# Kernel tuning notes

Hardware: AMD Instinct MI355X
Metric: run time of the kernel (lower is better)

The kernel has to match this reference:

```python
import jax, jax.numpy as jnp
import numpy as np

B, S, D_IN = 2, 2048, 2048
D_OUT, H, RD, L = 2048, 16, 64, 512
HD = D_OUT // H  # 128
ROPE_BASE = 10000.0
EPS = 1e-6


def _rmsnorm(x, w):
    # RMSNorm over last dim
    ms = jnp.mean(jnp.square(x), axis=-1, keepdims=True)
    return x * jax.lax.rsqrt(ms + EPS) * w


def _apply_rope(x, offset):
    # x: [B, H, T, RD]; GPT-NeoX style rotary embedding
    T, rd = x.shape[-2], x.shape[-1]
    pos = (offset + jnp.arange(T)).astype(jnp.float32)  # [T]
    inv_freq = 1.0 / (ROPE_BASE ** (jnp.arange(0, rd, 2, dtype=jnp.float32) / rd))  # [rd/2]
    ang = pos[:, None] * inv_freq[None, :]              # [T, rd/2]
    cos = jnp.cos(jnp.concatenate([ang, ang], axis=-1))  # [T, rd]
    sin = jnp.sin(jnp.concatenate([ang, ang], axis=-1))
    x1, x2 = jnp.split(x, 2, axis=-1)
    rot = jnp.concatenate([-x2, x1], axis=-1)
    return x * cos + rot * sin


def setup_inputs() -> dict:
    key = jax.random.key(0)
    ks = jax.random.split(key, 8)
    sc = 0.02
    return {
        "x": jax.random.normal(ks[0], (B, S, D_IN), jnp.float32),
        "W_DKV": jax.random.normal(ks[1], (L, D_IN), jnp.float32) * sc,
        "W_KRope": jax.random.normal(ks[2], (H * RD, D_IN), jnp.float32) * sc,
        "W_Q": jax.random.normal(ks[3], (D_OUT + H * RD, D_IN), jnp.float32) * sc,
        "W_UK": jax.random.normal(ks[4], (D_OUT, L), jnp.float32) * sc,
        "W_UV": jax.random.normal(ks[5], (D_OUT, L), jnp.float32) * sc,
        "W_O": jax.random.normal(ks[6], (D_IN, D_OUT), jnp.float32) * sc,
        "kv_norm_w": jnp.ones((L,), jnp.float32),
        "offset": 0,
    }


def reference(x, W_DKV, W_KRope, W_Q, W_UK, W_UV, W_O, kv_norm_w, offset):
    b, s, _ = x.shape
    # compressed latent KV (shared across heads)
    c_kv = _rmsnorm(x @ W_DKV.T, kv_norm_w)                      # [B,S,L]
    k_rope = (x @ W_KRope.T).reshape(b, s, H, RD).transpose(0, 2, 1, 3)  # [B,H,S,RD]
    # eval path: fused query projection
    q_total = x @ W_Q.T                                          # [B,S,D_OUT+H*RD]
    q_content = q_total[..., :D_OUT].reshape(b, s, H, HD).transpose(0, 2, 1, 3)  # [B,H,S,HD]
    q_rope = q_total[..., D_OUT:].reshape(b, s, H, RD).transpose(0, 2, 1, 3)     # [B,H,S,RD]
    q_rope = _apply_rope(q_rope, offset)
    k_rope = _apply_rope(k_rope, offset)
    # absorb W_UK into query: q_abs[b,h,s,l]
    w_uk = W_UK.reshape(H, HD, L)
    q_abs = jnp.einsum('bhsd,hdl->bhsl', q_content, w_uk)
    # attention scores against the shared latent + per-head rope keys
    scores = (jnp.einsum('bhsl,btl->bhst', q_abs, c_kv)
              + jnp.einsum('bhsr,bhtr->bhst', q_rope, k_rope))
    scores = scores * jax.lax.rsqrt(jnp.float32(HD + RD))
    t = c_kv.shape[1]
    causal = jnp.arange(t)[None, :] > (jnp.arange(s)[:, None] + offset)  # [S,T]
    scores = jnp.where(causal[None, None], -jnp.inf, scores)
    attn = jax.nn.softmax(scores, axis=-1)                       # [B,H,S,T]
    # attend in latent space, then absorb W_UV on the way out
    ctx_lat = jnp.einsum('bhst,btl->bhsl', attn, c_kv)           # [B,H,S,L]
    w_uv = W_UV.reshape(H, HD, L)
    ctx = jnp.einsum('bhsl,hdl->bhsd', ctx_lat, w_uv)            # [B,H,S,HD]
    ctx = ctx.transpose(0, 2, 1, 3).reshape(b, s, D_OUT)
    return ctx @ W_O.T
```

## Files before the change

### kernel.cpp

```cpp
#include <hip/hip_runtime.h>
#include <hip/hip_bf16.h>
#include <math.h>

#define B_    2
#define S_    2048
#define DIN   2048
#define DOUT  2048
#define H_    16
#define RD_   64
#define L_    512
#define HD_   128
#define BS_   (B_*S_)

typedef __attribute__((ext_vector_type(8))) short bf16x8;
typedef __attribute__((ext_vector_type(4))) float f32x4;

__device__ __forceinline__ short f2bs(float f) {
    __hip_bfloat16 h = __float2bfloat16(f);
    return *reinterpret_cast<short*>(&h);
}
__device__ __forceinline__ float bs2f(short s) {
    unsigned u = ((unsigned)(unsigned short)s) << 16;
    return __uint_as_float(u);
}

__device__ __forceinline__ void gld16(const void* g, void* l) {
    __builtin_amdgcn_global_load_lds(
        (const __attribute__((address_space(1))) unsigned int*)g,
        (__attribute__((address_space(3))) unsigned int*)l, 16, 0, 0);
}

__global__ __launch_bounds__(256) void cast_all(
    const float* __restrict__ x,    const float* __restrict__ wq,
    const float* __restrict__ wkr,  const float* __restrict__ wdkv,
    const float* __restrict__ wo,   const float* __restrict__ wuk,
    const float* __restrict__ wuv,
    short* __restrict__ x_bf,   short* __restrict__ wqkr_bf,
    short* __restrict__ wdkv_bf, short* __restrict__ wo_bf,
    short* __restrict__ wuk_bf,  short* __restrict__ wuv_bf)
{
    long long i = (long long)blockIdx.x * 256 + threadIdx.x;
    const float* src; short* dst; long long off;
    if      (i < 1048576) { src = x;    dst = x_bf;              off = i; }
    else if (i < 1835008) { src = wq;   dst = wqkr_bf;           off = i - 1048576; }
    else if (i < 2097152) { src = wkr;  dst = wqkr_bf + 6291456; off = i - 1835008; }
    else if (i < 2228224) { src = wdkv; dst = wdkv_bf;           off = i - 2097152; }
    else if (i < 2752512) { src = wo;   dst = wo_bf;             off = i - 2228224; }
    else if (i < 2883584) { src = wuk;  dst = wuk_bf;            off = i - 2752512; }
    else                  { src = wuv;  dst = wuv_bf;            off = i - 2883584; }
    float4 a = ((const float4*)src)[off*2], b = ((const float4*)src)[off*2+1];
    bf16x8 t;
    t[0]=f2bs(a.x); t[1]=f2bs(a.y); t[2]=f2bs(a.z); t[3]=f2bs(a.w);
    t[4]=f2bs(b.x); t[5]=f2bs(b.y); t[6]=f2bs(b.z); t[7]=f2bs(b.w);
    ((bf16x8*)dst)[off] = t;
}

__global__ __launch_bounds__(256, 4) void gemm_bf(
    const short* __restrict__ A, const short* __restrict__ Bw,
    float* __restrict__ Cf, short* __restrict__ Cb, int N, int K,
    long long az, long long bz, long long cz)
{
    const int z = blockIdx.z;
    A  += (long long)z * az;
    Bw += (long long)z * bz;
    if (Cf) Cf += (long long)z * cz; else Cb += (long long)z * cz;

    __shared__ short As[128*32];
    __shared__ short Bs[128*32];
    const int tid = threadIdx.x;
    const int m0 = blockIdx.y << 7, n0 = blockIdx.x << 7;
    const int w = tid >> 6, lane = tid & 63;
    const int quad = lane >> 4, n16 = lane & 15;
    const int mw = (w & 1) << 6, nw = (w >> 1) << 6;
    const int lr = lane >> 2, cg = lane & 3;
    const int swr = (quad ^ (n16 & 3)) << 3;

    f32x4 acc[4][4];
    #pragma unroll
    for (int mt = 0; mt < 4; mt++)
        #pragma unroll
        for (int nt = 0; nt < 4; nt++) acc[mt][nt] = (f32x4){0.f,0.f,0.f,0.f};

    for (int k0 = 0; k0 < K; k0 += 32) {
        #pragma unroll
        for (int jj = 0; jj < 2; jj++) {
            int rb = (jj*4 + w)*16;
            int r = rb + lr;
            int sc = (cg ^ (r & 3)) << 3;
            gld16(A  + (long long)(m0 + r)*K + k0 + sc, (void*)(As + rb*32));
            gld16(Bw + (long long)(n0 + r)*K + k0 + sc, (void*)(Bs + rb*32));
        }
        __syncthreads();
        bf16x8 af[4], bfr[4];
        #pragma unroll
        for (int t = 0; t < 4; t++) {
            af[t]  = *(const bf16x8*)(As + (mw + t*16 + n16)*32 + swr);
            bfr[t] = *(const bf16x8*)(Bs + (nw + t*16 + n16)*32 + swr);
        }
        #pragma unroll
        for (int mt = 0; mt < 4; mt++)
            #pragma unroll
            for (int nt = 0; nt < 4; nt++)
                acc[mt][nt] = __builtin_amdgcn_mfma_f32_16x16x32_bf16(
                                  af[mt], bfr[nt], acc[mt][nt], 0, 0, 0);
        __syncthreads();
    }

    #pragma unroll
    for (int mt = 0; mt < 4; mt++)
        #pragma unroll
        for (int nt = 0; nt < 4; nt++)
            #pragma unroll
            for (int r = 0; r < 4; r++) {
                long long row = m0 + mw + mt*16 + quad*4 + r;
                int col = n0 + nw + nt*16 + n16;
                if (Cf) Cf[row*(long long)N + col] = acc[mt][nt][r];
                else    Cb[row*(long long)N + col] = f2bs(acc[mt][nt][r]);
            }
}

__global__ __launch_bounds__(256) void rmsnorm_bf(const float* __restrict__ ckv,
                                                  const float* __restrict__ w,
                                                  short* __restrict__ out)
{
    const int row = blockIdx.x;
    const int tid = threadIdx.x;
    const float* p = ckv + (long long)row * L_;
    float v0 = p[tid], v1 = p[tid + 256];
    float ss = v0 * v0 + v1 * v1;
    #pragma unroll
    for (int o = 32; o >= 1; o >>= 1) ss += __shfl_xor(ss, o);
    __shared__ float wsum[4];
    if ((tid & 63) == 0) wsum[tid >> 6] = ss;
    __syncthreads();
    float tot = wsum[0] + wsum[1] + wsum[2] + wsum[3];
    float scale = rsqrtf(tot * (1.0f / (float)L_) + 1e-6f);
    out[(long long)row * L_ + tid]       = f2bs(v0 * scale * w[tid]);
    out[(long long)row * L_ + tid + 256] = f2bs(v1 * scale * w[tid + 256]);
}

__global__ __launch_bounds__(256) void rope_kernel(short* __restrict__ qkr,
                                                   const int* __restrict__ offp)
{
    const int offset = offp[0];
    long long idx = (long long)blockIdx.x * 256 + threadIdx.x;
    int r = (int)(idx & 31);
    long long t = idx >> 5;
    int h = (int)(t % H_);
    long long m = t / H_;
    int s = (int)(m % S_);

    float inv = __expf(-0.28782314f * (float)r);
    float ang = (float)(offset + s) * inv;
    float sn, cs;
    sincosf(ang, &sn, &cs);

    short* q = qkr + m * 4096 + 2048 + h * RD_;
    float x1 = bs2f(q[r]), x2 = bs2f(q[r + 32]);
    q[r]      = f2bs(x1 * cs - x2 * sn);
    q[r + 32] = f2bs(x2 * cs + x1 * sn);

    short* kk = qkr + m * 4096 + 3072 + h * RD_;
    x1 = bs2f(kk[r]); x2 = bs2f(kk[r + 32]);
    kk[r]      = f2bs(x1 * cs - x2 * sn);
    kk[r + 32] = f2bs(x2 * cs + x1 * sn);
}

#define SBUF 20480
#define TPP0 61440

__global__ __launch_bounds__(512)
__attribute__((amdgpu_waves_per_eu(2, 2)))
void flash_mha(
    const short* __restrict__ qkr,
    const short* __restrict__ K_up,
    const short* __restrict__ V_upT,
    const int* __restrict__ offp,
    short* __restrict__ ctx_bf)
{
    __shared__ short lds[70656];
    const int offset = offp[0];
    const int bh = blockIdx.y;
    const int b = bh >> 4, h = bh & 15;
    const int r0 = (int)(gridDim.x - 1 - blockIdx.x) * 128;
    const int tid = threadIdx.x;
    const int w = tid >> 6, lane = tid & 63;
    const int quad = lane >> 4, n16 = lane & 15;
    const int rx3 = (n16 & 7) << 3;
    const float scale = rsqrtf((float)(HD_ + RD_));

    const int l4 = lane >> 4, g16 = lane & 15;
    const int l8 = lane >> 3, g8 = lane & 7;

    const short* kc_src = K_up  + ((long long)b*S_)*2048 + h*HD_;
    const short* kr_src = qkr   + ((long long)b*S_)*4096 + 3072 + h*RD_;
    const short* vt_src = V_upT + ((long long)(b*S_ + h*HD_))*2048;

    auto stage = [&](int tk, int bi) {
        short* base = lds + bi*SBUF;
        #pragma unroll
        for (int j = 0; j < 2; j++) {
            int r4 = (w*2 + j)*4;
            int row = r4 + l4;
            int gs = g16 ^ (row & 7);
            gld16(kc_src + (long long)(tk + row)*2048 + gs*8,
                  (void*)(base + r4*128));
        }
        {
            int row = w*8 + l8;
            int gs = g8 ^ (l8 & 7);
            gld16(kr_src + (long long)(tk + row)*4096 + gs*8,
                  (void*)(base + 8192 + w*512));
        }
        #pragma unroll
        for (int j = 0; j < 2; j++) {
            int d8 = (w*2 + j)*8;
            int d = d8 + l8;
            int gs = g8 ^ (l8 & 7);
            gld16(vt_src + (long long)d*2048 + tk + gs*8,
                  (void*)(base + 12288 + d8*64));
        }
    };

    bf16x8 qf[6];
    {
        const short* qp = qkr + ((long long)(b*S_ + r0 + w*16 + n16))*4096;
        #pragma unroll
        for (int ks = 0; ks < 4; ks++)
            qf[ks] = *(const bf16x8*)(qp + h*HD_ + ks*32 + quad*8);
        qf[4] = *(const bf16x8*)(qp + 2048 + h*RD_ + quad*8);
        qf[5] = *(const bf16x8*)(qp + 2048 + h*RD_ + 32 + quad*8);
    }

    int tmax = r0 + 128 + offset;
    if (tmax > S_) tmax = S_;

    stage(0, 0);
    stage(64, 1);

    f32x4 Oacc[8];
    #pragma unroll
    for (int v = 0; v < 8; v++) Oacc[v] = (f32x4){0.f,0.f,0.f,0.f};
    float mrun[4] = {-INFINITY,-INFINITY,-INFINITY,-INFINITY};
    float lrun[4] = {0.f,0.f,0.f,0.f};

    int bi = 0;
    for (int t0 = 0; t0 < tmax; t0 += 64) {
        if (t0 + 64 < tmax) asm volatile("s_waitcnt vmcnt(5)" ::: "memory");
        else                asm volatile("s_waitcnt vmcnt(0)" ::: "memory");
        __builtin_amdgcn_s_barrier();
        __builtin_amdgcn_sched_barrier(0);

        {
            int bi2 = bi + 2; if (bi2 >= 3) bi2 -= 3;
            if (t0 + 128 < tmax) stage(t0 + 128, bi2);
        }

        const short* kcb = lds + bi*SBUF;
        const short* krb = kcb + 8192;
        const short* vtb = kcb + 12288;

        f32x4 Sf[4];
        #pragma unroll
        for (int nt = 0; nt < 4; nt++) {
            f32x4 a = {0.f,0.f,0.f,0.f};
            const short* kc = kcb + (nt*16 + n16)*128;
            #pragma unroll
            for (int ks = 0; ks < 4; ks++)
                a = __builtin_amdgcn_mfma_f32_16x16x32_bf16(
                        qf[ks], *(const bf16x8*)(kc + ((ks*32 + quad*8) ^ rx3)),
                        a, 0, 0, 0);
            const short* kr = krb + (nt*16 + n16)*64;
            a = __builtin_amdgcn_mfma_f32_16x16x32_bf16(
                    qf[4], *(const bf16x8*)(kr + ((quad*8) ^ rx3)), a, 0, 0, 0);
            a = __builtin_amdgcn_mfma_f32_16x16x32_bf16(
                    qf[5], *(const bf16x8*)(kr + ((32 + quad*8) ^ rx3)), a, 0, 0, 0);
            Sf[nt] = a;
        }

        float e0[4][4], lm[4];
        #pragma unroll
        for (int r = 0; r < 4; r++) {
            const int srow = r0 + w*16 + quad*4 + r;
            lm[r] = -INFINITY;
            #pragma unroll
            for (int nt = 0; nt < 4; nt++) {
                int t = t0 + nt*16 + n16;
                float s = (t <= srow + offset) ? Sf[nt][r]*scale : -INFINITY;
                e0[r][nt] = s;
                lm[r] = fmaxf(lm[r], s);
            }
        }
        bool trig = (lm[0] > mrun[0] + 8.f) | (lm[1] > mrun[1] + 8.f)
                  | (lm[2] > mrun[2] + 8.f) | (lm[3] > mrun[3] + 8.f);
        if (__any((int)trig)) {
            float al[4];
            #pragma unroll
            for (int r = 0; r < 4; r++) {
                float tm = lm[r];
                tm = fmaxf(tm, __shfl_xor(tm, 1));
                tm = fmaxf(tm, __shfl_xor(tm, 2));
                tm = fmaxf(tm, __shfl_xor(tm, 4));
                tm = fmaxf(tm, __shfl_xor(tm, 8));
                if (tm > mrun[r]) { al[r] = __expf(mrun[r] - tm); mrun[r] = tm; }
                else al[r] = 1.f;
            }
            #pragma unroll
            for (int v = 0; v < 8; v++) {
                Oacc[v][0] *= al[0]; Oacc[v][1] *= al[1];
                Oacc[v][2] *= al[2]; Oacc[v][3] *= al[3];
            }
            lrun[0] *= al[0]; lrun[1] *= al[1];
            lrun[2] *= al[2]; lrun[3] *= al[3];
        }
        #pragma unroll
        for (int r = 0; r < 4; r++) {
            float ps = 0.f;
            #pragma unroll
            for (int nt = 0; nt < 4; nt++) {
                float ex = __expf(e0[r][nt] - mrun[r]);
                ps += ex;
                lds[TPP0 + w*1152 + (quad*4 + r)*72 + nt*16 + n16] = f2bs(ex);
            }
            lrun[r] += ps;
        }

        bf16x8 pf0 = *(const bf16x8*)(lds + TPP0 + w*1152 + n16*72 + quad*8);
        bf16x8 pf1 = *(const bf16x8*)(lds + TPP0 + w*1152 + n16*72 + 32 + quad*8);
        const int vo0 = (quad*8) ^ rx3, vo1 = (32 + quad*8) ^ rx3;
        #pragma unroll
        for (int v = 0; v < 8; v++) {
            const short* vb = vtb + (v*16 + n16)*64;
            Oacc[v] = __builtin_amdgcn_mfma_f32_16x16x32_bf16(
                          pf0, *(const bf16x8*)(vb + vo0), Oacc[v], 0, 0, 0);
            Oacc[v] = __builtin_amdgcn_mfma_f32_16x16x32_bf16(
                          pf1, *(const bf16x8*)(vb + vo1), Oacc[v], 0, 0, 0);
        }

        bi = bi + 1; if (bi >= 3) bi = 0;
    }

    float inv[4];
    #pragma unroll
    for (int r = 0; r < 4; r++) {
        float s = lrun[r];
        s += __shfl_xor(s, 1);
        s += __shfl_xor(s, 2);
        s += __shfl_xor(s, 4);
        s += __shfl_xor(s, 8);
        inv[r] = 1.0f / s;
    }
    #pragma unroll
    for (int v = 0; v < 8; v++)
        #pragma unroll
        for (int r = 0; r < 4; r++) {
            long long row = (long long)b*S_ + r0 + w*16 + quad*4 + r;
            ctx_bf[row*2048 + h*HD_ + v*16 + n16] = f2bs(Oacc[v][r]*inv[r]);
        }
}

extern "C" void kernel_launch(void* const* d_in, const int* in_sizes, int n_in,
                              void* d_out, int out_size, void* d_ws, size_t ws_size,
                              hipStream_t stream)
{
    const float* x       = (const float*)d_in[0];
    const float* W_DKV   = (const float*)d_in[1];
    const float* W_KRope = (const float*)d_in[2];
    const float* W_Q     = (const float*)d_in[3];
    const float* W_UK    = (const float*)d_in[4];
    const float* W_UV    = (const float*)d_in[5];
    const float* W_O     = (const float*)d_in[6];
    const float* kvnw    = (const float*)d_in[7];
    const int*   offp    = (const int*)d_in[8];
    float* out = (float*)d_out;

    float* ws = (float*)d_ws;
    float* c_kv    = ws;
    short* x_bf    = (short*)(c_kv + 2097152);
    short* qkr_bf  = x_bf    + 8388608;
    short* c_kv_bf = qkr_bf  + 16777216;
    short* wuk_bf  = c_kv_bf + 2097152;
    short* wuv_bf  = wuk_bf  + 1048576;
    short* wdkv_bf = wuv_bf  + 1048576;
    short* wqkr_bf = wdkv_bf + 1048576;
    short* wo_bf   = wqkr_bf + 8388608;
    short* ctx_bf  = wo_bf   + 4194304;
    short* V_upT   = ctx_bf  + 8388608;
    short* K_up    = x_bf;

    dim3 blk(256);

    cast_all<<<11776, blk, 0, stream>>>(
        x, W_Q, W_KRope, W_DKV, W_O, W_UK, W_UV,
        x_bf, wqkr_bf, wdkv_bf, wo_bf, wuk_bf, wuv_bf);

    gemm_bf<<<dim3(32, 32), blk, 0, stream>>>(
        x_bf, wqkr_bf, nullptr, qkr_bf, 4096, 2048, 0, 0, 0);
    gemm_bf<<<dim3(4, 32), blk, 0, stream>>>(
        x_bf, wdkv_bf, c_kv, nullptr, 512, 2048, 0, 0, 0);
    rmsnorm_bf<<<4096, blk, 0, stream>>>(c_kv, kvnw, c_kv_bf);

    gemm_bf<<<dim3(16, 32), blk, 0, stream>>>(
        c_kv_bf, wuk_bf, nullptr, K_up, 2048, 512, 0, 0, 0);
    gemm_bf<<<dim3(16, 16, 2), blk, 0, stream>>>(
        wuv_bf, c_kv_bf, nullptr, V_upT, 2048, 512,
        0, (long long)S_*512, (long long)S_*2048);

    rope_kernel<<<8192, blk, 0, stream>>>(qkr_bf, offp);

    flash_mha<<<dim3(S_/128, B_*H_), dim3(512), 0, stream>>>(
        qkr_bf, K_up, V_upT, offp, ctx_bf);

    gemm_bf<<<dim3(16, 32), blk, 0, stream>>>(
        ctx_bf, wo_bf, out, nullptr, 2048, 2048, 0, 0, 0);
}
```

Measured before the change: 474.9 us.

## Shrink flash attention tiles to 64 queries and 32 keys with double-buffered LDS

The attention kernel now uses 256-thread blocks covering 64 query rows, walking keys in 32-wide steps. It replaces the triple-buffered LDS staging with a smaller double-buffered scheme that refills the buffer just consumed, behind an extra barrier. It also adds a fast path that skips causal masking on tiles that are entirely below the diagonal. The smaller footprint is meant to let more blocks run per CU and give finer causal granularity, at the cost of more loop iterations, more barriers and less prefetch depth.

```diff
diff --git a/kernel.cpp b/kernel.cpp
--- a/kernel.cpp
+++ b/kernel.cpp
@@ -166,11 +166,12 @@
     kk[r + 32] = f2bs(x2 * cs + x1 * sn);
 }
 
-#define SBUF 20480
-#define TPP0 61440
-
-__global__ __launch_bounds__(512)
-__attribute__((amdgpu_waves_per_eu(2, 2)))
+#define SB    10240
+#define KROFF 4096
+#define VOFF  6144
+#define PPO   20480
+
+__global__ __launch_bounds__(256, 3)
 void flash_mha(
     const short* __restrict__ qkr,
     const short* __restrict__ K_up,
@@ -178,26 +179,28 @@
     const int* __restrict__ offp,
     short* __restrict__ ctx_bf)
 {
-    __shared__ short lds[70656];
+    __shared__ short lds[23040];
     const int offset = offp[0];
     const int bh = blockIdx.y;
     const int b = bh >> 4, h = bh & 15;
-    const int r0 = (int)(gridDim.x - 1 - blockIdx.x) * 128;
+    const int r0 = (int)(gridDim.x - 1 - blockIdx.x) * 64;
     const int tid = threadIdx.x;
     const int w = tid >> 6, lane = tid & 63;
     const int quad = lane >> 4, n16 = lane & 15;
     const int rx3 = (n16 & 7) << 3;
+    const int vx3 = (n16 & 3) << 3;
     const float scale = rsqrtf((float)(HD_ + RD_));
 
     const int l4 = lane >> 4, g16 = lane & 15;
-    const int l8 = lane >> 3, g8 = lane & 7;
+    const int l8 = lane >> 3, g8  = lane & 7;
+    const int l2 = lane >> 2, g4  = lane & 3;
 
     const short* kc_src = K_up  + ((long long)b*S_)*2048 + h*HD_;
     const short* kr_src = qkr   + ((long long)b*S_)*4096 + 3072 + h*RD_;
     const short* vt_src = V_upT + ((long long)(b*S_ + h*HD_))*2048;
 
     auto stage = [&](int tk, int bi) {
-        short* base = lds + bi*SBUF;
+        short* base = lds + bi*SB;
         #pragma unroll
         for (int j = 0; j < 2; j++) {
             int r4 = (w*2 + j)*4;
@@ -208,17 +211,16 @@
         }
         {
             int row = w*8 + l8;
-            int gs = g8 ^ (l8 & 7);
-            gld16(kr_src + (long long)(tk + row)*4096 + gs*8,
-                  (void*)(base + 8192 + w*512));
+            gld16(kr_src + (long long)(tk + row)*4096 + (g8 ^ l8)*8,
+                  (void*)(base + KROFF + w*512));
         }
         #pragma unroll
         for (int j = 0; j < 2; j++) {
-            int d8 = (w*2 + j)*8;
-            int d = d8 + l8;
-            int gs = g8 ^ (l8 & 7);
+            int d16 = (w*2 + j)*16;
+            int d = d16 + l2;
+            int gs = g4 ^ (d & 3);
             gld16(vt_src + (long long)d*2048 + tk + gs*8,
-                  (void*)(base + 12288 + d8*64));
+                  (void*)(base + VOFF + d16*32));
         }
     };
 
@@ -232,11 +234,11 @@
         qf[5] = *(const bf16x8*)(qp + 2048 + h*RD_ + 32 + quad*8);
     }
 
-    int tmax = r0 + 128 + offset;
+    int tmax = r0 + 64 + offset;
     if (tmax > S_) tmax = S_;
 
     stage(0, 0);
-    stage(64, 1);
+    stage(32, 1);
 
     f32x4 Oacc[8];
     #pragma unroll
@@ -245,24 +247,19 @@
     float lrun[4] = {0.f,0.f,0.f,0.f};
 
     int bi = 0;
-    for (int t0 = 0; t0 < tmax; t0 += 64) {
-        if (t0 + 64 < tmax) asm volatile("s_waitcnt vmcnt(5)" ::: "memory");
+    for (int t0 = 0; t0 < tmax; t0 += 32) {
+        if (t0 + 32 < tmax) asm volatile("s_waitcnt vmcnt(5)" ::: "memory");
         else                asm volatile("s_waitcnt vmcnt(0)" ::: "memory");
         __builtin_amdgcn_s_barrier();
         __builtin_amdgcn_sched_barrier(0);
 
-        {
-            int bi2 = bi + 2; if (bi2 >= 3) bi2 -= 3;
-            if (t0 + 128 < tmax) stage(t0 + 128, bi2);
-        }
-
-        const short* kcb = lds + bi*SBUF;
-        const short* krb = kcb + 8192;
-        const short* vtb = kcb + 12288;
-
-        f32x4 Sf[4];
-        #pragma unroll
-        for (int nt = 0; nt < 4; nt++) {
+        const short* kcb = lds + bi*SB;
+        const short* krb = kcb + KROFF;
+        const short* vtb = kcb + VOFF;
+
+        f32x4 Sf[2];
+        #pragma unroll
+        for (int nt = 0; nt < 2; nt++) {
             f32x4 a = {0.f,0.f,0.f,0.f};
             const short* kc = kcb + (nt*16 + n16)*128;
             #pragma unroll
@@ -278,17 +275,27 @@
             Sf[nt] = a;
         }
 
-        float e0[4][4], lm[4];
-        #pragma unroll
-        for (int r = 0; r < 4; r++) {
-            const int srow = r0 + w*16 + quad*4 + r;
-            lm[r] = -INFINITY;
-            #pragma unroll
-            for (int nt = 0; nt < 4; nt++) {
-                int t = t0 + nt*16 + n16;
-                float s = (t <= srow + offset) ? Sf[nt][r]*scale : -INFINITY;
-                e0[r][nt] = s;
-                lm[r] = fmaxf(lm[r], s);
+        float e0[4][2], lm[4];
+        const bool full = (t0 + 31 <= r0 + w*16 + offset);
+        if (full) {
+            #pragma unroll
+            for (int r = 0; r < 4; r++) {
+                float s0 = Sf[0][r]*scale, s1 = Sf[1][r]*scale;
+                e0[r][0] = s0; e0[r][1] = s1;
+                lm[r] = fmaxf(s0, s1);
+            }
+        } else {
+            #pragma unroll
+            for (int r = 0; r < 4; r++) {
+                const int srow = r0 + w*16 + quad*4 + r;
+                lm[r] = -INFINITY;
+                #pragma unroll
+                for (int nt = 0; nt < 2; nt++) {
+                    int t = t0 + nt*16 + n16;
+                    float s = (t <= srow + offset) ? Sf[nt][r]*scale : -INFINITY;
+                    e0[r][nt] = s;
+                    lm[r] = fmaxf(lm[r], s);
+                }
             }
         }
         bool trig = (lm[0] > mrun[0] + 8.f) | (lm[1] > mrun[1] + 8.f)
@@ -317,27 +324,26 @@
         for (int r = 0; r < 4; r++) {
             float ps = 0.f;
             #pragma unroll
-            for (int nt = 0; nt < 4; nt++) {
+            for (int nt = 0; nt < 2; nt++) {
                 float ex = __expf(e0[r][nt] - mrun[r]);
                 ps += ex;
-                lds[TPP0 + w*1152 + (quad*4 + r)*72 + nt*16 + n16] = f2bs(ex);
+                lds[PPO + w*640 + (quad*4 + r)*40 + nt*16 + n16] = f2bs(ex);
             }
             lrun[r] += ps;
         }
 
-        bf16x8 pf0 = *(const bf16x8*)(lds + TPP0 + w*1152 + n16*72 + quad*8);
-        bf16x8 pf1 = *(const bf16x8*)(lds + TPP0 + w*1152 + n16*72 + 32 + quad*8);
-        const int vo0 = (quad*8) ^ rx3, vo1 = (32 + quad*8) ^ rx3;
+        bf16x8 pf = *(const bf16x8*)(lds + PPO + w*640 + n16*40 + quad*8);
+        const int vo = (quad*8) ^ vx3;
         #pragma unroll
         for (int v = 0; v < 8; v++) {
-            const short* vb = vtb + (v*16 + n16)*64;
+            const short* vb = vtb + (v*16 + n16)*32;
             Oacc[v] = __builtin_amdgcn_mfma_f32_16x16x32_bf16(
-                          pf0, *(const bf16x8*)(vb + vo0), Oacc[v], 0, 0, 0);
-            Oacc[v] = __builtin_amdgcn_mfma_f32_16x16x32_bf16(
-                          pf1, *(const bf16x8*)(vb + vo1), Oacc[v], 0, 0, 0);
-        }
-
-        bi = bi + 1; if (bi >= 3) bi = 0;
+                          pf, *(const bf16x8*)(vb + vo), Oacc[v], 0, 0, 0);
+        }
+
+        __builtin_amdgcn_s_barrier();
+        if (t0 + 64 < tmax) stage(t0 + 64, bi);
+        bi ^= 1;
     }
 
     float inv[4];
@@ -408,7 +414,7 @@
 
     rope_kernel<<<8192, blk, 0, stream>>>(qkr_bf, offp);
 
-    flash_mha<<<dim3(S_/128, B_*H_), dim3(512), 0, stream>>>(
+    flash_mha<<<dim3(S_/64, B_*H_), dim3(256), 0, stream>>>(
         qkr_bf, K_up, V_upT, offp, ctx_bf);
 
     gemm_bf<<<dim3(16, 32), blk, 0, stream>>>(
```

Result: slower. 505.2 us (+6.4%).
